# Performance work log

Measured on AMD Instinct MI355X. Metric: run time of the kernel, lower is better.

## Reference

```python
import jax, jax.numpy as jnp
import numpy as np

COORD = 5.0
NOOBJ = 0.5


def _reflat(x):
    # torch: flatten(x.transpose(0,1), start_dim=1).transpose(0,1) -> [B*S*S, C]
    C = x.shape[1]
    return jnp.moveaxis(x, 1, -1).reshape(-1, C)


def setup_inputs() -> dict:
    key = jax.random.key(0)
    k1, k2 = jax.random.split(key)
    B, C, S = 256, 25, 64
    inp = jax.random.uniform(k1, (B, C, S, S), dtype=jnp.float32)
    tgt = jax.random.uniform(k2, (B, C, S, S), dtype=jnp.float32)
    return {"input": inp, "target": tgt}


def _iou(b1, b2, blocks):
    # vectorized, detached IoU between predicted and target boxes, per row
    b1 = jax.lax.stop_gradient(b1)
    b2 = jax.lax.stop_gradient(b2)
    c1 = b1[:, :2] / blocks
    c2 = b2[:, :2] / blocks
    x1a, x2a = c1[:, 0] - b1[:, 2] / 2, c1[:, 0] + b1[:, 2] / 2
    y1a, y2a = c1[:, 1] - b1[:, 3] / 2, c1[:, 1] + b1[:, 3] / 2
    x1b, x2b = c2[:, 0] - b2[:, 2] / 2, c2[:, 0] + b2[:, 2] / 2
    y1b, y2b = c2[:, 1] - b2[:, 3] / 2, c2[:, 1] + b2[:, 3] / 2
    dx = jnp.minimum(x2a, x2b) - jnp.maximum(x1a, x1b)
    dy = jnp.minimum(y2a, y2b) - jnp.maximum(y1a, y1b)
    inter = dx * dy
    union = b1[:, 2] * b1[:, 3] + b2[:, 2] * b2[:, 3] - inter
    pos = (dx > 0) & (dy > 0)
    return jnp.where(pos, inter / jnp.where(pos, union, 1.0), 0.0)


def reference(input, target):
    blocks = target.shape[-1]
    t = _reflat(target)  # [N, C]
    p = _reflat(input)   # [N, C]
    m = (t[:, 4] > 0).astype(p.dtype)  # responsible-cell mask [N]
    iou = _iou(p[:, :4], t[:, :4], blocks)  # detached target confidence
    sp = jnp.sqrt(p[:, 2:4])
    st = jnp.sqrt(t[:, 2:4])
    m2 = m[:, None]
    loss = COORD * jnp.sum(m2 * jnp.square(p[:, :2] - t[:, :2]))
    loss += COORD * jnp.sum(m2 * jnp.square(sp - st))
    loss += jnp.sum(m * jnp.square(p[:, 4] - iou))
    loss += NOOBJ * jnp.sum((1.0 - m) * jnp.square(p[:, 4]))
    loss += jnp.sum(m2 * jnp.square(p[:, 5:] - t[:, 5:]))
    return loss
```

## Files before the change

### kernel.cpp

```cpp
#include <hip/hip_runtime.h>


#define COORD 5.0f
#define NOOBJ 0.5f

constexpr int B = 256;
constexpr int C = 25;
constexpr int S = 64;
constexpr int SS = S * S;
constexpr int CH_STRIDE4 = SS / 4;
constexpr int IMG_STRIDE4 = C * CH_STRIDE4;
constexpr int N4 = B * SS / 4;

__device__ __forceinline__ float comp(const float4 v, int k) {
    switch (k) {
        case 0: return v.x;
        case 1: return v.y;
        case 2: return v.z;
        default: return v.w;
    }
}

__global__ void zero_out_kernel(float* out) { out[0] = 0.0f; }

__global__ __launch_bounds__(256) void yolo_loss_kernel(
        const float4* __restrict__ in, const float4* __restrict__ tg,
        float* __restrict__ out) {
    const int g = blockIdx.x * blockDim.x + threadIdx.x;
    float acc = 0.0f;
    if (g < N4) {
        const int b = g >> 10;
        const int pp = g & 1023;
        const int base = b * IMG_STRIDE4 + pp;

        float4 p0 = in[base + 0 * CH_STRIDE4];
        float4 p1 = in[base + 1 * CH_STRIDE4];
        float4 p2 = in[base + 2 * CH_STRIDE4];
        float4 p3 = in[base + 3 * CH_STRIDE4];
        float4 p4 = in[base + 4 * CH_STRIDE4];
        float4 t0 = tg[base + 0 * CH_STRIDE4];
        float4 t1 = tg[base + 1 * CH_STRIDE4];
        float4 t2 = tg[base + 2 * CH_STRIDE4];
        float4 t3 = tg[base + 3 * CH_STRIDE4];
        float4 t4 = tg[base + 4 * CH_STRIDE4];

        float mv[4];
        const float invBlocks = 1.0f / (float)S;

        #pragma unroll
        for (int k = 0; k < 4; ++k) {
            const float px = comp(p0, k), py = comp(p1, k);
            const float pw = comp(p2, k), ph = comp(p3, k);
            const float pc = comp(p4, k);
            const float tx = comp(t0, k), ty = comp(t1, k);
            const float tw = comp(t2, k), th = comp(t3, k);
            const float tc = comp(t4, k);
            const float m = (tc > 0.0f) ? 1.0f : 0.0f;
            mv[k] = m;

            const float c1x = px * invBlocks, c1y = py * invBlocks;
            const float c2x = tx * invBlocks, c2y = ty * invBlocks;
            const float x1a = c1x - pw * 0.5f, x2a = c1x + pw * 0.5f;
            const float y1a = c1y - ph * 0.5f, y2a = c1y + ph * 0.5f;
            const float x1b = c2x - tw * 0.5f, x2b = c2x + tw * 0.5f;
            const float y1b = c2y - th * 0.5f, y2b = c2y + th * 0.5f;
            const float dx = fminf(x2a, x2b) - fmaxf(x1a, x1b);
            const float dy = fminf(y2a, y2b) - fmaxf(y1a, y1b);
            const float inter = dx * dy;
            const float uni = pw * ph + tw * th - inter;
            const bool pos = (dx > 0.0f) && (dy > 0.0f);
            const float iou = pos ? (inter / uni) : 0.0f;

            const float ex = px - tx, ey = py - ty;
            acc += COORD * m * (ex * ex + ey * ey);
            const float sw = sqrtf(pw) - sqrtf(tw);
            const float sh = sqrtf(ph) - sqrtf(th);
            acc += COORD * m * (sw * sw + sh * sh);
            const float ec = pc - iou;
            acc += m * ec * ec;
            acc += NOOBJ * (1.0f - m) * (pc * pc);
        }

        #pragma unroll
        for (int c = 5; c < 25; ++c) {
            const float4 pv = in[base + c * CH_STRIDE4];
            const float4 tv = tg[base + c * CH_STRIDE4];
            float d;
            d = pv.x - tv.x; acc += mv[0] * d * d;
            d = pv.y - tv.y; acc += mv[1] * d * d;
            d = pv.z - tv.z; acc += mv[2] * d * d;
            d = pv.w - tv.w; acc += mv[3] * d * d;
        }
    }

    #pragma unroll
    for (int off = 32; off > 0; off >>= 1)
        acc += __shfl_down(acc, off, 64);

    __shared__ float smem[4];
    const int lane = threadIdx.x & 63;
    const int wid = threadIdx.x >> 6;
    if (lane == 0) smem[wid] = acc;
    __syncthreads();
    if (threadIdx.x == 0) {
        const float s = smem[0] + smem[1] + smem[2] + smem[3];
        atomicAdd(out, s);
    }
}

extern "C" void kernel_launch(void* const* d_in, const int* in_sizes, int n_in,
                              void* d_out, int out_size, void* d_ws, size_t ws_size,
                              hipStream_t stream) {
    const float4* in = (const float4*)d_in[0];
    const float4* tg = (const float4*)d_in[1];
    float* out = (float*)d_out;

    zero_out_kernel<<<1, 1, 0, stream>>>(out);

    const int threads = 256;
    const int blocks = (N4 + threads - 1) / threads;
    yolo_loss_kernel<<<blocks, threads, 0, stream>>>(in, tg, out);
}
```

Baseline: 222.7 us.

## Split channel work across five block groups to raise parallelism

Each position is now processed by five blocks: one computes box/IoU/confidence terms from channels 0-4, and four others each handle five class channels, reloading the mask channel. This raises the number of blocks and memory-level parallelism per thread so the memory-bound reduction can keep more loads in flight. In exchange it rereads the target confidence channel four extra times, adds more atomics, and creates load imbalance between groups.

```diff
diff --git a/kernel.cpp b/kernel.cpp
--- a/kernel.cpp
+++ b/kernel.cpp
@@ -10,29 +10,25 @@
 constexpr int SS = S * S;
 constexpr int CH_STRIDE4 = SS / 4;
 constexpr int IMG_STRIDE4 = C * CH_STRIDE4;
-constexpr int N4 = B * SS / 4;
-
-__device__ __forceinline__ float comp(const float4 v, int k) {
-    switch (k) {
-        case 0: return v.x;
-        case 1: return v.y;
-        case 2: return v.z;
-        default: return v.w;
-    }
-}
+constexpr int NPOS4 = B * SS / 4;
+constexpr int BLOCKS_PER_GROUP = NPOS4 / 256;
+constexpr int NGROUPS = 5;
 
 __global__ void zero_out_kernel(float* out) { out[0] = 0.0f; }
 
 __global__ __launch_bounds__(256) void yolo_loss_kernel(
         const float4* __restrict__ in, const float4* __restrict__ tg,
         float* __restrict__ out) {
-    const int g = blockIdx.x * blockDim.x + threadIdx.x;
+    const int group = blockIdx.x % NGROUPS;
+    const int chunk = blockIdx.x / NGROUPS;
+    const int gpos = (chunk << 8) | threadIdx.x;
+    const int b = gpos >> 10;
+    const int pp = gpos & 1023;
+    const int base = b * IMG_STRIDE4 + pp;
+
     float acc = 0.0f;
-    if (g < N4) {
-        const int b = g >> 10;
-        const int pp = g & 1023;
-        const int base = b * IMG_STRIDE4 + pp;
 
+    if (group == 0) {
         float4 p0 = in[base + 0 * CH_STRIDE4];
         float4 p1 = in[base + 1 * CH_STRIDE4];
         float4 p2 = in[base + 2 * CH_STRIDE4];
@@ -44,19 +40,24 @@
         float4 t3 = tg[base + 3 * CH_STRIDE4];
         float4 t4 = tg[base + 4 * CH_STRIDE4];
 
-        float mv[4];
         const float invBlocks = 1.0f / (float)S;
+        float px4[4] = {p0.x, p0.y, p0.z, p0.w};
+        float py4[4] = {p1.x, p1.y, p1.z, p1.w};
+        float pw4[4] = {p2.x, p2.y, p2.z, p2.w};
+        float ph4[4] = {p3.x, p3.y, p3.z, p3.w};
+        float pc4[4] = {p4.x, p4.y, p4.z, p4.w};
+        float tx4[4] = {t0.x, t0.y, t0.z, t0.w};
+        float ty4[4] = {t1.x, t1.y, t1.z, t1.w};
+        float tw4[4] = {t2.x, t2.y, t2.z, t2.w};
+        float th4[4] = {t3.x, t3.y, t3.z, t3.w};
+        float tc4[4] = {t4.x, t4.y, t4.z, t4.w};
 
         #pragma unroll
         for (int k = 0; k < 4; ++k) {
-            const float px = comp(p0, k), py = comp(p1, k);
-            const float pw = comp(p2, k), ph = comp(p3, k);
-            const float pc = comp(p4, k);
-            const float tx = comp(t0, k), ty = comp(t1, k);
-            const float tw = comp(t2, k), th = comp(t3, k);
-            const float tc = comp(t4, k);
-            const float m = (tc > 0.0f) ? 1.0f : 0.0f;
-            mv[k] = m;
+            const float px = px4[k], py = py4[k], pw = pw4[k], ph = ph4[k];
+            const float pc = pc4[k];
+            const float tx = tx4[k], ty = ty4[k], tw = tw4[k], th = th4[k];
+            const float m = (tc4[k] > 0.0f) ? 1.0f : 0.0f;
 
             const float c1x = px * invBlocks, c1y = py * invBlocks;
             const float c2x = tx * invBlocks, c2y = ty * invBlocks;
@@ -80,17 +81,29 @@
             acc += m * ec * ec;
             acc += NOOBJ * (1.0f - m) * (pc * pc);
         }
-
+    } else {
+        const int c0 = 5 + (group - 1) * 5;
+        float4 t4 = tg[base + 4 * CH_STRIDE4];
+        float4 pv[5], tv[5];
         #pragma unroll
-        for (int c = 5; c < 25; ++c) {
-            const float4 pv = in[base + c * CH_STRIDE4];
-            const float4 tv = tg[base + c * CH_STRIDE4];
+        for (int j = 0; j < 5; ++j) {
+            pv[j] = in[base + (c0 + j) * CH_STRIDE4];
+            tv[j] = tg[base + (c0 + j) * CH_STRIDE4];
+        }
+        const float m0 = (t4.x > 0.0f) ? 1.0f : 0.0f;
+        const float m1 = (t4.y > 0.0f) ? 1.0f : 0.0f;
+        const float m2 = (t4.z > 0.0f) ? 1.0f : 0.0f;
+        const float m3 = (t4.w > 0.0f) ? 1.0f : 0.0f;
+        float a0 = 0.0f, a1 = 0.0f, a2 = 0.0f, a3 = 0.0f;
+        #pragma unroll
+        for (int j = 0; j < 5; ++j) {
             float d;
-            d = pv.x - tv.x; acc += mv[0] * d * d;
-            d = pv.y - tv.y; acc += mv[1] * d * d;
-            d = pv.z - tv.z; acc += mv[2] * d * d;
-            d = pv.w - tv.w; acc += mv[3] * d * d;
+            d = pv[j].x - tv[j].x; a0 += d * d;
+            d = pv[j].y - tv[j].y; a1 += d * d;
+            d = pv[j].z - tv[j].z; a2 += d * d;
+            d = pv[j].w - tv[j].w; a3 += d * d;
         }
+        acc = m0 * a0 + m1 * a1 + m2 * a2 + m3 * a3;
     }
 
     #pragma unroll
@@ -118,6 +131,6 @@
     zero_out_kernel<<<1, 1, 0, stream>>>(out);
 
     const int threads = 256;
-    const int blocks = (N4 + threads - 1) / threads;
+    const int blocks = BLOCKS_PER_GROUP * NGROUPS;
     yolo_loss_kernel<<<blocks, threads, 0, stream>>>(in, tg, out);
 }
```

Measured after the change: 226.4 us. Within noise of the previous version (+1.7%).

## Remap threads over flat channel-plane index space with per-element mask reloads

Applied to the files above, without the earlier changes.

Instead of each thread loading all 25 channels for four pixels, threads now walk the flat float4 index space of the input tensors, each processing four elements from different grid-strided blocks. Per-channel work is selected by the channel index: coordinate/size/class channels reload the mask from channel 4, and the confidence channel reloads the four box channels to compute IoU. This aims to make memory access contiguous and increase parallelism and occupancy. The cost is redundant reads of the mask and box channels, which rely on cache hits.

```diff
diff --git a/kernel.cpp b/kernel.cpp
--- a/kernel.cpp
+++ b/kernel.cpp
@@ -5,91 +5,83 @@
 #define NOOBJ 0.5f
 
 constexpr int B = 256;
-constexpr int C = 25;
 constexpr int S = 64;
 constexpr int SS = S * S;
-constexpr int CH_STRIDE4 = SS / 4;
-constexpr int IMG_STRIDE4 = C * CH_STRIDE4;
-constexpr int N4 = B * SS / 4;
-
-__device__ __forceinline__ float comp(const float4 v, int k) {
-    switch (k) {
-        case 0: return v.x;
-        case 1: return v.y;
-        case 2: return v.z;
-        default: return v.w;
-    }
-}
+constexpr int CH4 = SS / 4;
+constexpr int NF4 = B * 25 * CH4;
+constexpr int THREADS = 256;
+constexpr int ITERS = 4;
+constexpr int BLOCKS = NF4 / (THREADS * ITERS);
 
 __global__ void zero_out_kernel(float* out) { out[0] = 0.0f; }
+
+__device__ __forceinline__ float conf_term(float px, float py, float pw, float ph,
+                                           float tx, float ty, float tw, float th,
+                                           float pc, float tc) {
+    const float inv = 1.0f / 64.0f;
+    const float m = (tc > 0.0f) ? 1.0f : 0.0f;
+    const float c1x = px * inv, c1y = py * inv;
+    const float c2x = tx * inv, c2y = ty * inv;
+    const float dx = fminf(c1x + pw * 0.5f, c2x + tw * 0.5f)
+                   - fmaxf(c1x - pw * 0.5f, c2x - tw * 0.5f);
+    const float dy = fminf(c1y + ph * 0.5f, c2y + th * 0.5f)
+                   - fmaxf(c1y - ph * 0.5f, c2y - th * 0.5f);
+    const float inter = dx * dy;
+    const float uni = pw * ph + tw * th - inter;
+    const bool pos = (dx > 0.0f) && (dy > 0.0f);
+    const float iou = pos ? (inter / uni) : 0.0f;
+    const float e = pc - iou;
+    return m * e * e + NOOBJ * (1.0f - m) * pc * pc;
+}
 
 __global__ __launch_bounds__(256) void yolo_loss_kernel(
         const float4* __restrict__ in, const float4* __restrict__ tg,
         float* __restrict__ out) {
-    const int g = blockIdx.x * blockDim.x + threadIdx.x;
     float acc = 0.0f;
-    if (g < N4) {
-        const int b = g >> 10;
+
+    #pragma unroll
+    for (int it = 0; it < ITERS; ++it) {
+        const int g = (it * BLOCKS + (int)blockIdx.x) * THREADS + (int)threadIdx.x;
+        const int plane = g >> 10;
         const int pp = g & 1023;
-        const int base = b * IMG_STRIDE4 + pp;
+        const int b = plane / 25;
+        const int c = plane - b * 25;
 
-        float4 p0 = in[base + 0 * CH_STRIDE4];
-        float4 p1 = in[base + 1 * CH_STRIDE4];
-        float4 p2 = in[base + 2 * CH_STRIDE4];
-        float4 p3 = in[base + 3 * CH_STRIDE4];
-        float4 p4 = in[base + 4 * CH_STRIDE4];
-        float4 t0 = tg[base + 0 * CH_STRIDE4];
-        float4 t1 = tg[base + 1 * CH_STRIDE4];
-        float4 t2 = tg[base + 2 * CH_STRIDE4];
-        float4 t3 = tg[base + 3 * CH_STRIDE4];
-        float4 t4 = tg[base + 4 * CH_STRIDE4];
+        const float4 p = in[g];
+        const float4 t = tg[g];
 
-        float mv[4];
-        const float invBlocks = 1.0f / (float)S;
-
-        #pragma unroll
-        for (int k = 0; k < 4; ++k) {
-            const float px = comp(p0, k), py = comp(p1, k);
-            const float pw = comp(p2, k), ph = comp(p3, k);
-            const float pc = comp(p4, k);
-            const float tx = comp(t0, k), ty = comp(t1, k);
-            const float tw = comp(t2, k), th = comp(t3, k);
-            const float tc = comp(t4, k);
-            const float m = (tc > 0.0f) ? 1.0f : 0.0f;
-            mv[k] = m;
-
-            const float c1x = px * invBlocks, c1y = py * invBlocks;
-            const float c2x = tx * invBlocks, c2y = ty * invBlocks;
-            const float x1a = c1x - pw * 0.5f, x2a = c1x + pw * 0.5f;
-            const float y1a = c1y - ph * 0.5f, y2a = c1y + ph * 0.5f;
-            const float x1b = c2x - tw * 0.5f, x2b = c2x + tw * 0.5f;
-            const float y1b = c2y - th * 0.5f, y2b = c2y + th * 0.5f;
-            const float dx = fminf(x2a, x2b) - fmaxf(x1a, x1b);
-            const float dy = fminf(y2a, y2b) - fmaxf(y1a, y1b);
-            const float inter = dx * dy;
-            const float uni = pw * ph + tw * th - inter;
-            const bool pos = (dx > 0.0f) && (dy > 0.0f);
-            const float iou = pos ? (inter / uni) : 0.0f;
-
-            const float ex = px - tx, ey = py - ty;
-            acc += COORD * m * (ex * ex + ey * ey);
-            const float sw = sqrtf(pw) - sqrtf(tw);
-            const float sh = sqrtf(ph) - sqrtf(th);
-            acc += COORD * m * (sw * sw + sh * sh);
-            const float ec = pc - iou;
-            acc += m * ec * ec;
-            acc += NOOBJ * (1.0f - m) * (pc * pc);
-        }
-
-        #pragma unroll
-        for (int c = 5; c < 25; ++c) {
-            const float4 pv = in[base + c * CH_STRIDE4];
-            const float4 tv = tg[base + c * CH_STRIDE4];
-            float d;
-            d = pv.x - tv.x; acc += mv[0] * d * d;
-            d = pv.y - tv.y; acc += mv[1] * d * d;
-            d = pv.z - tv.z; acc += mv[2] * d * d;
-            d = pv.w - tv.w; acc += mv[3] * d * d;
+        if (c == 4) {
+            const int base0 = ((b * 25) << 10) | pp;
+            const float4 p0 = in[base0 + 0 * CH4];
+            const float4 p1 = in[base0 + 1 * CH4];
+            const float4 p2 = in[base0 + 2 * CH4];
+            const float4 p3 = in[base0 + 3 * CH4];
+            const float4 t0 = tg[base0 + 0 * CH4];
+            const float4 t1 = tg[base0 + 1 * CH4];
+            const float4 t2 = tg[base0 + 2 * CH4];
+            const float4 t3 = tg[base0 + 3 * CH4];
+            acc += conf_term(p0.x, p1.x, p2.x, p3.x, t0.x, t1.x, t2.x, t3.x, p.x, t.x);
+            acc += conf_term(p0.y, p1.y, p2.y, p3.y, t0.y, t1.y, t2.y, t3.y, p.y, t.y);
+            acc += conf_term(p0.z, p1.z, p2.z, p3.z, t0.z, t1.z, t2.z, t3.z, p.z, t.z);
+            acc += conf_term(p0.w, p1.w, p2.w, p3.w, t0.w, t1.w, t2.w, t3.w, p.w, t.w);
+        } else {
+            const int mbase = ((b * 25 + 4) << 10) | pp;
+            const float4 mk = tg[mbase];
+            const float w = (c < 4) ? COORD : 1.0f;
+            const bool dos = (c == 2) || (c == 3);
+            float pv[4] = {p.x, p.y, p.z, p.w};
+            float tv[4] = {t.x, t.y, t.z, t.w};
+            const float mv[4] = {mk.x > 0.0f ? 1.0f : 0.0f,
+                                 mk.y > 0.0f ? 1.0f : 0.0f,
+                                 mk.z > 0.0f ? 1.0f : 0.0f,
+                                 mk.w > 0.0f ? 1.0f : 0.0f};
+            #pragma unroll
+            for (int k = 0; k < 4; ++k) {
+                float a = pv[k], bb = tv[k];
+                if (dos) { a = sqrtf(a); bb = sqrtf(bb); }
+                const float d = a - bb;
+                acc += w * mv[k] * d * d;
+            }
         }
     }
 
@@ -117,7 +109,5 @@
 
     zero_out_kernel<<<1, 1, 0, stream>>>(out);
 
-    const int threads = 256;
-    const int blocks = (N4 + threads - 1) / threads;
-    yolo_loss_kernel<<<blocks, threads, 0, stream>>>(in, tg, out);
+    yolo_loss_kernel<<<BLOCKS, THREADS, 0, stream>>>(in, tg, out);
 }
```

Result: slower. 248.5 us (+11.5%).
